# Performance work log

Hardware: AMD Instinct MI355X
Metric: run time of the kernel (lower is better)

## Reference

```python
import jax, jax.numpy as jnp
import numpy as np

B, NV, JN = 1024, 8, 21
V = NV * JN            # 168 tokens = num_view * joint_num
F_DIM, NH, DQ, DV = 512, 4, 128, 128
HID = 512
EPS = 1e-6
NEG = float(-2**32 + 1)


def _layer_norm(x, g, b):
    mu = jnp.mean(x, axis=-1, keepdims=True)
    var = jnp.mean(jnp.square(x - mu), axis=-1, keepdims=True)
    return (x - mu) * jax.lax.rsqrt(var + EPS) * g + b


def setup_inputs() -> dict:
    key = jax.random.key(0)
    ks = jax.random.split(key, 12)
    s = 0.02
    return {
        "x": jax.random.normal(ks[0], (B, V, F_DIM), dtype=jnp.float32),
        "valid": jax.random.randint(ks[1], (B, NV), 0, 2),
        "wq": jax.random.normal(ks[2], (NH * DQ, F_DIM), dtype=jnp.float32) * s,
        "bq": jnp.zeros((NH * DQ,), dtype=jnp.float32),
        "wk": jax.random.normal(ks[3], (NH * DQ, F_DIM), dtype=jnp.float32) * s,
        "bk": jnp.zeros((NH * DQ,), dtype=jnp.float32),
        "wv": jax.random.normal(ks[4], (NH * DV, F_DIM), dtype=jnp.float32) * s,
        "bv": jnp.zeros((NH * DV,), dtype=jnp.float32),
        "fc_w": jax.random.normal(ks[5], (F_DIM, NH * DV), dtype=jnp.float32) * s,
        "fc_b": jnp.zeros((F_DIM,), dtype=jnp.float32),
        "ln1_g": jnp.ones((F_DIM,), dtype=jnp.float32),
        "ln1_b": jnp.zeros((F_DIM,), dtype=jnp.float32),
        "ln2_g": jnp.ones((F_DIM,), dtype=jnp.float32),
        "ln2_b": jnp.zeros((F_DIM,), dtype=jnp.float32),
        "fc1_w": jax.random.normal(ks[6], (HID, F_DIM), dtype=jnp.float32) * s,
        "fc1_b": jnp.zeros((HID,), dtype=jnp.float32),
        "fc2_w": jax.random.normal(ks[7], (F_DIM, HID), dtype=jnp.float32) * s,
        "fc2_b": jnp.zeros((F_DIM,), dtype=jnp.float32),
    }


def reference(x, valid, wq, bq, wk, bk, wv, bv, fc_w, fc_b,
              ln1_g, ln1_b, ln2_g, ln2_b, fc1_w, fc1_b, fc2_w, fc2_b):
    bs = x.shape[0]
    h = _layer_norm(x, ln1_g, ln1_b)                          # [B,V,f]
    q = (h @ wq.T + bq).reshape(bs, V, NH, DQ)                # [B,V,H,dq]
    k = (h @ wk.T + bk).reshape(bs, V, NH, DQ)
    v = (h @ wv.T + bv).reshape(bs, V, NH, DV)
    attn = jnp.einsum('bqhd,bkhd->bhqk', q, k) / jnp.sqrt(jnp.float32(DQ))
    # valid mask: per-view validity expanded to per-token, pairwise additive
    w = jnp.where(valid == 0, NEG, 0.0).astype(x.dtype)       # [B,NV]
    w = jnp.repeat(w, JN, axis=1)                             # [B,V], view-major
    m = w[:, :, None] + w[:, None, :]                         # [B,V,V]
    attn = attn + m[:, None, :, :]
    attn = jax.nn.softmax(attn, axis=-1)
    out = jnp.einsum('bhqk,bkhd->bqhd', attn, v).reshape(bs, V, NH * DV)
    out = out @ fc_w.T + fc_b
    x = x + out
    # MLP residual block
    h2 = _layer_norm(x, ln2_g, ln2_b)
    h2 = jax.nn.relu(h2 @ fc1_w.T + fc1_b) @ fc2_w.T + fc2_b
    return x + h2
```

## Files before the change

kernel.cpp:

```cpp
#include <hip/hip_runtime.h>
#include <stdint.h>

#define BATCH 1024
#define NVIEW 8
#define JN_   21
#define VTOK  168
#define FDIM  512
#define NHEAD 4
#define DHEAD 128
#define MROWS (BATCH*VTOK)
#define SCALE2 0.127517434f

typedef __attribute__((ext_vector_type(8))) short s8v;
typedef __attribute__((ext_vector_type(4))) short s4v;
typedef __attribute__((ext_vector_type(4))) float f4v;

static __device__ __forceinline__ short f2bf(float f){
  unsigned u = __builtin_bit_cast(unsigned, f);
  unsigned r = (u + 0x7FFFu + ((u >> 16) & 1u)) >> 16;
  return (short)(unsigned short)r;
}
static __device__ __forceinline__ float bf2f(short s){
  unsigned u = ((unsigned)(unsigned short)s) << 16;
  return __builtin_bit_cast(float, u);
}

#define GL16(gp, lp) __builtin_amdgcn_global_load_lds( \
    (__attribute__((address_space(1))) void*)(gp), \
    (__attribute__((address_space(3))) void*)(lp), 16, 0, 0)

__global__ __launch_bounds__(256) void convert_w(
    const float* __restrict__ wq, const float* __restrict__ wk,
    const float* __restrict__ wv, const float* __restrict__ fcw,
    const float* __restrict__ fc1, const float* __restrict__ fc2,
    short* __restrict__ dst){
  int id = blockIdx.x * 256 + threadIdx.x;
  int e = id * 4;
  int seg = e >> 18;
  int off = e & 262143;
  const float* s = seg==0?wq: seg==1?wk: seg==2?wv: seg==3?fcw: seg==4?fc1: fc2;
  float4 u = *(const float4*)(s + off);
  s4v o; o[0]=f2bf(u.x); o[1]=f2bf(u.y); o[2]=f2bf(u.z); o[3]=f2bf(u.w);
  *(s4v*)(dst + e) = o;
}

__global__ __launch_bounds__(256) void ln1_kernel(
    const float* __restrict__ x, const float* __restrict__ g,
    const float* __restrict__ bb, short* __restrict__ h){
  int row  = blockIdx.x * 4 + (threadIdx.x >> 6);
  int lane = threadIdx.x & 63;
  size_t base = (size_t)row * 512 + lane * 8;
  float4 u0 = *(const float4*)(x + base);
  float4 u1 = *(const float4*)(x + base + 4);
  float s = u0.x+u0.y+u0.z+u0.w + u1.x+u1.y+u1.z+u1.w;
  float q = u0.x*u0.x+u0.y*u0.y+u0.z*u0.z+u0.w*u0.w
          + u1.x*u1.x+u1.y*u1.y+u1.z*u1.z+u1.w*u1.w;
  #pragma unroll
  for (int o = 1; o < 64; o <<= 1){ s += __shfl_xor(s,o); q += __shfl_xor(q,o); }
  float mu = s * (1.f/512.f);
  float rstd = rsqrtf(q*(1.f/512.f) - mu*mu + 1e-6f);
  float4 g0 = *(const float4*)(g + lane*8),  g1 = *(const float4*)(g + lane*8 + 4);
  float4 b0 = *(const float4*)(bb + lane*8), b1 = *(const float4*)(bb + lane*8 + 4);
  s8v o_;
  o_[0]=f2bf((u0.x-mu)*rstd*g0.x+b0.x); o_[1]=f2bf((u0.y-mu)*rstd*g0.y+b0.y);
  o_[2]=f2bf((u0.z-mu)*rstd*g0.z+b0.z); o_[3]=f2bf((u0.w-mu)*rstd*g0.w+b0.w);
  o_[4]=f2bf((u1.x-mu)*rstd*g1.x+b1.x); o_[5]=f2bf((u1.y-mu)*rstd*g1.y+b1.y);
  o_[6]=f2bf((u1.z-mu)*rstd*g1.z+b1.z); o_[7]=f2bf((u1.w-mu)*rstd*g1.w+b1.w);
  *(s8v*)(h + base) = o_;
}

__global__ __launch_bounds__(256) void resid_ln(
    const float* __restrict__ x, const short* __restrict__ y,
    const float* __restrict__ g, const float* __restrict__ bb,
    short* __restrict__ g2){
  int row  = blockIdx.x * 4 + (threadIdx.x >> 6);
  int lane = threadIdx.x & 63;
  size_t base = (size_t)row * 512 + lane * 8;
  float4 u0 = *(const float4*)(x + base);
  float4 u1 = *(const float4*)(x + base + 4);
  s8v yv = *(const s8v*)(y + base);
  float v[8];
  v[0]=u0.x+bf2f(yv[0]); v[1]=u0.y+bf2f(yv[1]); v[2]=u0.z+bf2f(yv[2]); v[3]=u0.w+bf2f(yv[3]);
  v[4]=u1.x+bf2f(yv[4]); v[5]=u1.y+bf2f(yv[5]); v[6]=u1.z+bf2f(yv[6]); v[7]=u1.w+bf2f(yv[7]);
  float s = 0.f, q = 0.f;
  #pragma unroll
  for (int i = 0; i < 8; i++){ s += v[i]; q += v[i]*v[i]; }
  #pragma unroll
  for (int o = 1; o < 64; o <<= 1){ s += __shfl_xor(s,o); q += __shfl_xor(q,o); }
  float mu = s * (1.f/512.f);
  float rstd = rsqrtf(q*(1.f/512.f) - mu*mu + 1e-6f);
  float4 g0 = *(const float4*)(g + lane*8),  g1 = *(const float4*)(g + lane*8 + 4);
  float4 b0 = *(const float4*)(bb + lane*8), b1 = *(const float4*)(bb + lane*8 + 4);
  s8v o_;
  o_[0]=f2bf((v[0]-mu)*rstd*g0.x+b0.x); o_[1]=f2bf((v[1]-mu)*rstd*g0.y+b0.y);
  o_[2]=f2bf((v[2]-mu)*rstd*g0.z+b0.z); o_[3]=f2bf((v[3]-mu)*rstd*g0.w+b0.w);
  o_[4]=f2bf((v[4]-mu)*rstd*g1.x+b1.x); o_[5]=f2bf((v[5]-mu)*rstd*g1.y+b1.y);
  o_[6]=f2bf((v[6]-mu)*rstd*g1.z+b1.z); o_[7]=f2bf((v[7]-mu)*rstd*g1.w+b1.w);
  *(s8v*)(g2 + base) = o_;
}

template<int MODE>
__global__ __launch_bounds__(512) void gemm_bt(
    const short* __restrict__ A, const short* __restrict__ Bm,
    const float* __restrict__ bias0, const float* __restrict__ bias1,
    const float* __restrict__ aux, short* __restrict__ out0,
    short* __restrict__ out1, float* __restrict__ outf){
  __shared__ short As[3][16384];
  __shared__ short Bs[3][8192];
  int tid = threadIdx.x, lane = tid & 63;
  int wid = tid >> 6, wr = wid >> 1, wc = wid & 1;
  int lg = lane >> 4, l15 = lane & 15;
  int nwg  = gridDim.x * gridDim.y;
  int flat = blockIdx.y * gridDim.x + blockIdx.x;
  int cpx  = nwg >> 3;
  int swz  = (flat & 7) * cpx + (flat >> 3);
  int bx = swz % gridDim.x, by = swz / gridDim.x;
  size_t mt, nt;
  if (MODE == 1){ mt = bx; nt = by; }
  else          { nt = bx; mt = by; }
  size_t m0 = mt * 256, n0 = nt * 128;
  const short* Ab = A + m0 * 512;
  const short* Bb = Bm + n0 * 512;
  f4v zf = {0.f,0.f,0.f,0.f};
  f4v acc[4][4];
  #pragma unroll
  for (int m=0;m<4;m++)
    #pragma unroll
    for (int n=0;n<4;n++) acc[m][n] = zf;

#define STAGE_T(bufi, kt) do {                                        \
    _Pragma("unroll")                                                 \
    for (int r_ = 0; r_ < 4; r_++){                                   \
      int c_ = r_*512 + tid;                                          \
      int row_ = c_ >> 3;                                             \
      int chk_ = (c_ & 7) ^ (row_ & 7);                               \
      GL16(Ab + (size_t)row_*512 + (kt) + chk_*8, &As[bufi][c_*8]);   \
    }                                                                 \
    _Pragma("unroll")                                                 \
    for (int r_ = 0; r_ < 2; r_++){                                   \
      int c_ = r_*512 + tid;                                          \
      int row_ = c_ >> 3;                                             \
      int chk_ = (c_ & 7) ^ (row_ & 7);                               \
      GL16(Bb + (size_t)row_*512 + (kt) + chk_*8, &Bs[bufi][c_*8]);   \
    }                                                                 \
  } while(0)

  STAGE_T(0, 0); STAGE_T(1, 64); STAGE_T(2, 128);

  #pragma unroll
  for (int t = 0; t < 8; ++t){
    if (t < 6)       asm volatile("s_waitcnt vmcnt(12)" ::: "memory");
    else if (t == 6) asm volatile("s_waitcnt vmcnt(6)"  ::: "memory");
    else             asm volatile("s_waitcnt vmcnt(0)"  ::: "memory");
    __builtin_amdgcn_s_barrier();
    __builtin_amdgcn_sched_barrier(0);
    {
      const short* Ap = As[t % 3];
      const short* Bp = Bs[t % 3];
      #pragma unroll
      for (int kk8 = 0; kk8 < 8; kk8 += 4){
        s8v af_[4], bf_[4];
        int pc_ = ((kk8 + lg) ^ (l15 & 7)) << 3;
        #pragma unroll
        for (int m_=0;m_<4;m_++) af_[m_] = *(const s8v*)&Ap[(wr*64+m_*16+l15)*64 + pc_];
        #pragma unroll
        for (int n_=0;n_<4;n_++) bf_[n_] = *(const s8v*)&Bp[(wc*64+n_*16+l15)*64 + pc_];
        __builtin_amdgcn_s_setprio(1);
        #pragma unroll
        for (int m_=0;m_<4;m_++)
          #pragma unroll
          for (int n_=0;n_<4;n_++)
            acc[m_][n_] = __builtin_amdgcn_mfma_f32_16x16x32_bf16(af_[m_], bf_[n_], acc[m_][n_], 0,0,0);
        __builtin_amdgcn_s_setprio(0);
      }
    }
    if (t < 5){
      __builtin_amdgcn_s_barrier();
      __builtin_amdgcn_sched_barrier(0);
      STAGE_T((t + 3) % 3, (t + 3) * 64);
    }
  }
#undef STAGE_T

  #pragma unroll
  for (int m=0;m<4;m++)
  #pragma unroll
  for (int n=0;n<4;n++)
  #pragma unroll
  for (int r=0;r<4;r++){
    int rowL = wr*64 + m*16 + lg*4 + r;
    int colL = wc*64 + n*16 + l15;
    size_t gm = m0 + rowL, gn = n0 + colL;
    float val = acc[m][n][r];
    if (MODE == 0){
      int nn = (int)gn;
      val += (nn < 512) ? bias0[nn] : bias1[nn - 512];
      int head = (nn >> 7) & 3, d = nn & 127;
      size_t b = gm / 168, tok = gm - b * 168;
      size_t idx = ((b*4 + head)*168 + tok)*128 + d;
      ((nn < 512) ? out0 : out1)[idx] = f2bf(val);
    } else if (MODE == 1){
      val += bias0[gm];
      int hh = ((int)gm >> 7) & 3, d = (int)gm & 127;
      size_t b = gn / 168, tok = gn - b * 168;
      out0[((b*4 + hh)*128 + d)*168 + tok] = f2bf(val);
    } else if (MODE == 2 || MODE == 3){
      val += bias0[gn];
      if (MODE == 3) val = fmaxf(val, 0.f);
      out0[gm*512 + gn] = f2bf(val);
    } else {
      val += bias0[gn] + aux[gm*512 + gn] + bf2f(out1[gm*512 + gn]);
      outf[gm*512 + gn] = val;
    }
  }
}

__global__ __launch_bounds__(256, 2) void attn_kernel(
    const short* __restrict__ qg_, const short* __restrict__ kg_,
    const short* __restrict__ vtg_, const int* __restrict__ valid,
    short* __restrict__ outp){
  __shared__ short Ps[192*200];

  int tid = threadIdx.x, lane = tid & 63, wid = tid >> 6;
  int lg = lane >> 4, l15 = lane & 15;
  int bh = blockIdx.x, b = bh >> 2, hh = bh & 3;
  const short* qg  = qg_  + (size_t)bh * (168*128);
  const short* kg  = kg_  + (size_t)bh * (168*128);
  const short* vtg = vtg_ + (size_t)bh * (128*168);

  int bits = 0;
  #pragma unroll
  for (int v = 0; v < 8; v++) bits |= (valid[b*8 + v] != 0) << v;
  if (bits == 0) bits = 255;
  float wk2[11];
  #pragma unroll
  for (int n = 0; n < 11; n++){
    int kt = n*16 + l15;
    int view = (kt * 781) >> 14;
    wk2[n] = ((bits >> view) & 1) ? 0.0f : -1.0e9f;
  }

  int row0 = wid * 48;
  f4v zf = {0.f,0.f,0.f,0.f};

  s8v qf[3][4];
  #pragma unroll
  for (int m=0;m<3;m++)
    #pragma unroll
    for (int kf=0;kf<4;kf++)
      qf[m][kf] = *(const s8v*)(qg + (size_t)(row0 + m*16 + l15)*128 + kf*32 + lg*8);

  f4v accS[3][11];
  #pragma unroll
  for (int m=0;m<3;m++)
    #pragma unroll
    for (int n=0;n<11;n++) accS[m][n] = zf;
  s8v kb[2][4];
  #pragma unroll
  for (int kf=0;kf<4;kf++)
    kb[0][kf] = *(const s8v*)(kg + (size_t)l15*128 + kf*32 + lg*8);
  #pragma unroll
  for (int n=0;n<11;n++){
    if (n < 10){
      #pragma unroll
      for (int kf=0;kf<4;kf++)
        kb[(n+1)&1][kf] = *(const s8v*)(kg + (size_t)((n+1)*16 + l15)*128 + kf*32 + lg*8);
    }
    __builtin_amdgcn_s_setprio(1);
    #pragma unroll
    for (int kf=0;kf<4;kf++)
      #pragma unroll
      for (int m=0;m<3;m++)
        accS[m][n] = __builtin_amdgcn_mfma_f32_16x16x32_bf16(qf[m][kf], kb[n&1][kf], accS[m][n], 0,0,0);
    __builtin_amdgcn_s_setprio(0);
  }

  float inv_[3][4];
  #pragma unroll
  for (int m=0;m<3;m++){
    #pragma unroll
    for (int r=0;r<4;r++){
      int qtok = row0 + m*16 + lg*4 + r;
      float sum = 0.f;
      #pragma unroll
      for (int n=0;n<11;n++){
        float p = exp2f(fmaf(accS[m][n][r], SCALE2, wk2[n]));
        sum += p;
        Ps[qtok*200 + n*16 + l15] = f2bf(p);
      }
      sum += __shfl_xor(sum,1); sum += __shfl_xor(sum,2);
      sum += __shfl_xor(sum,4); sum += __shfl_xor(sum,8);
      inv_[m][r] = 1.0f / sum;
    }
  }
  {
    s8v z8 = {0,0,0,0,0,0,0,0};
    for (int i = lane; i < 96; i += 64){
      int rr = row0 + (i >> 1);
      *(s8v*)&Ps[rr*200 + 176 + (i&1)*8] = z8;
    }
  }

  s8v ap[3][6];
  #pragma unroll
  for (int m=0;m<3;m++)
    #pragma unroll
    for (int kf=0;kf<6;kf++)
      ap[m][kf] = *(const s8v*)&Ps[(row0 + m*16 + l15)*200 + kf*32 + lg*8];

  f4v accO[3][8];
  #pragma unroll
  for (int m=0;m<3;m++)
    #pragma unroll
    for (int n=0;n<8;n++) accO[m][n] = zf;
  s8v vb[2][6];
  #pragma unroll
  for (int kf=0;kf<6;kf++)
    vb[0][kf] = *(const s8v*)(vtg + (size_t)l15*168 + kf*32 + lg*8);
  #pragma unroll
  for (int n=0;n<8;n++){
    if (n < 7){
      #pragma unroll
      for (int kf=0;kf<6;kf++)
        vb[(n+1)&1][kf] = *(const s8v*)(vtg + (size_t)((n+1)*16 + l15)*168 + kf*32 + lg*8);
    }
    __builtin_amdgcn_s_setprio(1);
    #pragma unroll
    for (int kf=0;kf<6;kf++)
      #pragma unroll
      for (int m=0;m<3;m++)
        accO[m][n] = __builtin_amdgcn_mfma_f32_16x16x32_bf16(ap[m][kf], vb[n&1][kf], accO[m][n], 0,0,0);
    __builtin_amdgcn_s_setprio(0);
  }

  #pragma unroll
  for (int m=0;m<3;m++){
    #pragma unroll
    for (int r=0;r<4;r++){
      int qtok = row0 + m*16 + lg*4 + r;
      if (qtok < 168){
        float iv = inv_[m][r];
        size_t base = ((size_t)b*168 + qtok)*512 + hh*128;
        #pragma unroll
        for (int n=0;n<8;n++)
          outp[base + n*16 + l15] = f2bf(accO[m][n][r] * iv);
      }
    }
  }
}

extern "C" void kernel_launch(void* const* d_in, const int* in_sizes, int n_in,
                              void* d_out, int out_size, void* d_ws, size_t ws_size,
                              hipStream_t stream) {
  const float* x     = (const float*)d_in[0];
  const int*   valid = (const int*)  d_in[1];
  const float* wq    = (const float*)d_in[2];
  const float* bq    = (const float*)d_in[3];
  const float* wk    = (const float*)d_in[4];
  const float* bk    = (const float*)d_in[5];
  const float* wv    = (const float*)d_in[6];
  const float* bv    = (const float*)d_in[7];
  const float* fcw   = (const float*)d_in[8];
  const float* fcb   = (const float*)d_in[9];
  const float* ln1g  = (const float*)d_in[10];
  const float* ln1b  = (const float*)d_in[11];
  const float* ln2g  = (const float*)d_in[12];
  const float* ln2b  = (const float*)d_in[13];
  const float* fc1w  = (const float*)d_in[14];
  const float* fc1b  = (const float*)d_in[15];
  const float* fc2w  = (const float*)d_in[16];
  const float* fc2b  = (const float*)d_in[17];

  char* ws = (char*)d_ws;
  short* h       = (short*)(ws + 0LL);
  short* q_ws    = (short*)(ws + 176160768LL);
  short* k_ws    = (short*)(ws + 352321536LL);
  short* vt_ws   = (short*)(ws + 528482304LL);
  short* wb      = (short*)(ws + 704643072LL);
  short* attn_o  = h;
  short* y       = q_ws;
  short* g2      = h;
  short* a1      = k_ws;
  float* outp    = (float*)d_out;

  convert_w<<<1536, 256, 0, stream>>>(wq, wk, wv, fcw, fc1w, fc2w, wb);
  ln1_kernel<<<MROWS/4, 256, 0, stream>>>(x, ln1g, ln1b, h);
  gemm_bt<0><<<dim3(8, MROWS/256), 512, 0, stream>>>(h, wb, bq, bk, nullptr, q_ws, k_ws, nullptr);
  gemm_bt<1><<<dim3(2, MROWS/128), 512, 0, stream>>>(wb + 524288, h, bv, nullptr, nullptr, vt_ws, nullptr, nullptr);
  attn_kernel<<<BATCH*NHEAD, 256, 0, stream>>>(q_ws, k_ws, vt_ws, valid, attn_o);
  gemm_bt<2><<<dim3(4, MROWS/256), 512, 0, stream>>>(attn_o, wb + 786432, fcb, nullptr, nullptr, y, nullptr, nullptr);
  resid_ln<<<MROWS/4, 256, 0, stream>>>(x, y, ln2g, ln2b, g2);
  gemm_bt<3><<<dim3(4, MROWS/256), 512, 0, stream>>>(g2, wb + 1048576, fc1b, nullptr, nullptr, a1, nullptr, nullptr);
  gemm_bt<4><<<dim3(4, MROWS/256), 512, 0, stream>>>(a1, wb + 1310720, fc2b, nullptr, (float*)x, nullptr, y, outp);
}
```

Measured before the change: 1.527 ms.

## Restructure GEMM pipeline to BK=32 triple-buffer, bf16 residual, deeper attention prefetch

The GEMM main loop moves from three 64-wide K stages with a split wait/stage schedule to sixteen 32-wide stages. Each stage loads its fragments, issues the next global-to-LDS copy, then runs MFMAs. LDS use drops so launch_bounds can request 4 blocks per SM. resid_ln now writes x+attn as bf16 so the final GEMM reads one bf16 residual instead of fp32 x plus bf16 y, cutting epilogue traffic at the cost of rounding the residual to bf16. The attention kernel's K and V fragment prefetch deepens from double to triple buffering, which costs more registers.

```diff
diff --git a/kernel.cpp b/kernel.cpp
--- a/kernel.cpp
+++ b/kernel.cpp
@@ -72,7 +72,7 @@
 __global__ __launch_bounds__(256) void resid_ln(
     const float* __restrict__ x, const short* __restrict__ y,
     const float* __restrict__ g, const float* __restrict__ bb,
-    short* __restrict__ g2){
+    short* __restrict__ x2b, short* __restrict__ g2){
   int row  = blockIdx.x * 4 + (threadIdx.x >> 6);
   int lane = threadIdx.x & 63;
   size_t base = (size_t)row * 512 + lane * 8;
@@ -82,6 +82,10 @@
   float v[8];
   v[0]=u0.x+bf2f(yv[0]); v[1]=u0.y+bf2f(yv[1]); v[2]=u0.z+bf2f(yv[2]); v[3]=u0.w+bf2f(yv[3]);
   v[4]=u1.x+bf2f(yv[4]); v[5]=u1.y+bf2f(yv[5]); v[6]=u1.z+bf2f(yv[6]); v[7]=u1.w+bf2f(yv[7]);
+  s8v xv;
+  #pragma unroll
+  for (int i = 0; i < 8; i++) xv[i] = f2bf(v[i]);
+  *(s8v*)(x2b + base) = xv;
   float s = 0.f, q = 0.f;
   #pragma unroll
   for (int i = 0; i < 8; i++){ s += v[i]; q += v[i]*v[i]; }
@@ -100,85 +104,76 @@
 }
 
 template<int MODE>
-__global__ __launch_bounds__(512) void gemm_bt(
+__global__ __launch_bounds__(512, 4) void gemm_bt(
     const short* __restrict__ A, const short* __restrict__ Bm,
     const float* __restrict__ bias0, const float* __restrict__ bias1,
-    const float* __restrict__ aux, short* __restrict__ out0,
+    const short* __restrict__ aux, short* __restrict__ out0,
     short* __restrict__ out1, float* __restrict__ outf){
-  __shared__ short As[3][16384];
-  __shared__ short Bs[3][8192];
-  int tid = threadIdx.x, lane = tid & 63;
-  int wid = tid >> 6, wr = wid >> 1, wc = wid & 1;
-  int lg = lane >> 4, l15 = lane & 15;
-  int nwg  = gridDim.x * gridDim.y;
-  int flat = blockIdx.y * gridDim.x + blockIdx.x;
-  int cpx  = nwg >> 3;
-  int swz  = (flat & 7) * cpx + (flat >> 3);
-  int bx = swz % gridDim.x, by = swz / gridDim.x;
+  __shared__ short lds[36864];
+  short* const AL = lds;
+  short* const BL = lds + 24576;
+  const int tid = threadIdx.x, lane = tid & 63;
+  const int wid = tid >> 6, wr = wid >> 1, wc = wid & 1;
+  const int lg = lane >> 4, l15 = lane & 15;
+  const int nwg  = gridDim.x * gridDim.y;
+  const int flat = blockIdx.y * gridDim.x + blockIdx.x;
+  const int swz  = (flat & 7) * (nwg >> 3) + (flat >> 3);
   size_t mt, nt;
-  if (MODE == 1){ mt = bx; nt = by; }
-  else          { nt = bx; mt = by; }
-  size_t m0 = mt * 256, n0 = nt * 128;
+  if (MODE == 1){ mt = swz & 1; nt = (size_t)(swz >> 1); }
+  else {
+    constexpr int GX = (MODE == 0) ? 8 : 4;
+    nt = swz % GX; mt = swz / GX;
+  }
+  const size_t m0 = mt * 256, n0 = nt * 128;
   const short* Ab = A + m0 * 512;
   const short* Bb = Bm + n0 * 512;
-  f4v zf = {0.f,0.f,0.f,0.f};
+
+#define STAGE_T(tt) do {                                                \
+    short* da_ = AL + ((tt)%3)*8192;                                    \
+    _Pragma("unroll")                                                   \
+    for (int r_ = 0; r_ < 2; r_++){                                     \
+      int c_ = r_*512 + tid;                                            \
+      int row_ = c_ >> 2, chk_ = (c_ & 3) ^ (row_ & 3);                 \
+      GL16(Ab + (size_t)row_*512 + (tt)*32 + chk_*8, da_ + c_*8);       \
+    }                                                                   \
+    {                                                                   \
+      short* db_ = BL + ((tt)%3)*4096;                                  \
+      int row_ = tid >> 2, chk_ = (tid & 3) ^ (row_ & 3);               \
+      GL16(Bb + (size_t)row_*512 + (tt)*32 + chk_*8, db_ + tid*8);      \
+    } } while(0)
+
+  STAGE_T(0); STAGE_T(1);
+  asm volatile("s_waitcnt vmcnt(3)" ::: "memory");
+  __builtin_amdgcn_s_barrier();
+
   f4v acc[4][4];
   #pragma unroll
   for (int m=0;m<4;m++)
     #pragma unroll
-    for (int n=0;n<4;n++) acc[m][n] = zf;
-
-#define STAGE_T(bufi, kt) do {                                        \
-    _Pragma("unroll")                                                 \
-    for (int r_ = 0; r_ < 4; r_++){                                   \
-      int c_ = r_*512 + tid;                                          \
-      int row_ = c_ >> 3;                                             \
-      int chk_ = (c_ & 7) ^ (row_ & 7);                               \
-      GL16(Ab + (size_t)row_*512 + (kt) + chk_*8, &As[bufi][c_*8]);   \
-    }                                                                 \
-    _Pragma("unroll")                                                 \
-    for (int r_ = 0; r_ < 2; r_++){                                   \
-      int c_ = r_*512 + tid;                                          \
-      int row_ = c_ >> 3;                                             \
-      int chk_ = (c_ & 7) ^ (row_ & 7);                               \
-      GL16(Bb + (size_t)row_*512 + (kt) + chk_*8, &Bs[bufi][c_*8]);   \
-    }                                                                 \
-  } while(0)
-
-  STAGE_T(0, 0); STAGE_T(1, 64); STAGE_T(2, 128);
-
-  #pragma unroll
-  for (int t = 0; t < 8; ++t){
-    if (t < 6)       asm volatile("s_waitcnt vmcnt(12)" ::: "memory");
-    else if (t == 6) asm volatile("s_waitcnt vmcnt(6)"  ::: "memory");
-    else             asm volatile("s_waitcnt vmcnt(0)"  ::: "memory");
+    for (int n=0;n<4;n++) acc[m][n] = f4v{0.f,0.f,0.f,0.f};
+
+  #pragma unroll
+  for (int t = 0; t < 16; ++t){
+    const short* Awp = AL + (t%3)*8192 + (wr*64 + l15)*32;
+    const short* Bwp = BL + (t%3)*4096 + (wc*64 + l15)*32;
+    const int cA = (lg ^ (l15 & 3)) * 8;
+    s8v af[4], bf[4];
+    #pragma unroll
+    for (int m=0;m<4;m++) af[m] = *(const s8v*)(Awp + m*512 + cA);
+    #pragma unroll
+    for (int n=0;n<4;n++) bf[n] = *(const s8v*)(Bwp + n*512 + cA);
+    if (t < 14) STAGE_T(t+2);
     __builtin_amdgcn_s_barrier();
-    __builtin_amdgcn_sched_barrier(0);
-    {
-      const short* Ap = As[t % 3];
-      const short* Bp = Bs[t % 3];
-      #pragma unroll
-      for (int kk8 = 0; kk8 < 8; kk8 += 4){
-        s8v af_[4], bf_[4];
-        int pc_ = ((kk8 + lg) ^ (l15 & 7)) << 3;
-        #pragma unroll
-        for (int m_=0;m_<4;m_++) af_[m_] = *(const s8v*)&Ap[(wr*64+m_*16+l15)*64 + pc_];
-        #pragma unroll
-        for (int n_=0;n_<4;n_++) bf_[n_] = *(const s8v*)&Bp[(wc*64+n_*16+l15)*64 + pc_];
-        __builtin_amdgcn_s_setprio(1);
-        #pragma unroll
-        for (int m_=0;m_<4;m_++)
-          #pragma unroll
-          for (int n_=0;n_<4;n_++)
-            acc[m_][n_] = __builtin_amdgcn_mfma_f32_16x16x32_bf16(af_[m_], bf_[n_], acc[m_][n_], 0,0,0);
-        __builtin_amdgcn_s_setprio(0);
-      }
-    }
-    if (t < 5){
-      __builtin_amdgcn_s_barrier();
-      __builtin_amdgcn_sched_barrier(0);
-      STAGE_T((t + 3) % 3, (t + 3) * 64);
-    }
+    __builtin_amdgcn_s_setprio(1);
+    #pragma unroll
+    for (int m=0;m<4;m++)
+      #pragma unroll
+      for (int n=0;n<4;n++)
+        acc[m][n] = __builtin_amdgcn_mfma_f32_16x16x32_bf16(af[m], bf[n], acc[m][n], 0,0,0);
+    __builtin_amdgcn_s_setprio(0);
+    if (t <= 13)      asm volatile("s_waitcnt vmcnt(3)" ::: "memory");
+    else if (t == 14) asm volatile("s_waitcnt vmcnt(0)" ::: "memory");
+    __builtin_amdgcn_s_barrier();
   }
 #undef STAGE_T
 
@@ -209,7 +204,7 @@
       if (MODE == 3) val = fmaxf(val, 0.f);
       out0[gm*512 + gn] = f2bf(val);
     } else {
-      val += bias0[gn] + aux[gm*512 + gn] + bf2f(out1[gm*512 + gn]);
+      val += bias0[gn] + bf2f(aux[gm*512 + gn]);
       outf[gm*512 + gn] = val;
     }
   }
@@ -255,23 +250,25 @@
   for (int m=0;m<3;m++)
     #pragma unroll
     for (int n=0;n<11;n++) accS[m][n] = zf;
-  s8v kb[2][4];
-  #pragma unroll
-  for (int kf=0;kf<4;kf++)
-    kb[0][kf] = *(const s8v*)(kg + (size_t)l15*128 + kf*32 + lg*8);
+  s8v kb[3][4];
+  #pragma unroll
+  for (int p=0;p<2;p++)
+    #pragma unroll
+    for (int kf=0;kf<4;kf++)
+      kb[p][kf] = *(const s8v*)(kg + (size_t)(p*16 + l15)*128 + kf*32 + lg*8);
   #pragma unroll
   for (int n=0;n<11;n++){
-    if (n < 10){
+    if (n < 9){
       #pragma unroll
       for (int kf=0;kf<4;kf++)
-        kb[(n+1)&1][kf] = *(const s8v*)(kg + (size_t)((n+1)*16 + l15)*128 + kf*32 + lg*8);
+        kb[(n+2)%3][kf] = *(const s8v*)(kg + (size_t)((n+2)*16 + l15)*128 + kf*32 + lg*8);
     }
     __builtin_amdgcn_s_setprio(1);
     #pragma unroll
     for (int kf=0;kf<4;kf++)
       #pragma unroll
       for (int m=0;m<3;m++)
-        accS[m][n] = __builtin_amdgcn_mfma_f32_16x16x32_bf16(qf[m][kf], kb[n&1][kf], accS[m][n], 0,0,0);
+        accS[m][n] = __builtin_amdgcn_mfma_f32_16x16x32_bf16(qf[m][kf], kb[n%3][kf], accS[m][n], 0,0,0);
     __builtin_amdgcn_s_setprio(0);
   }
 
@@ -313,23 +310,25 @@
   for (int m=0;m<3;m++)
     #pragma unroll
     for (int n=0;n<8;n++) accO[m][n] = zf;
-  s8v vb[2][6];
-  #pragma unroll
-  for (int kf=0;kf<6;kf++)
-    vb[0][kf] = *(const s8v*)(vtg + (size_t)l15*168 + kf*32 + lg*8);
+  s8v vb[3][6];
+  #pragma unroll
+  for (int p=0;p<2;p++)
+    #pragma unroll
+    for (int kf=0;kf<6;kf++)
+      vb[p][kf] = *(const s8v*)(vtg + (size_t)(p*16 + l15)*168 + kf*32 + lg*8);
   #pragma unroll
   for (int n=0;n<8;n++){
-    if (n < 7){
+    if (n < 6){
       #pragma unroll
       for (int kf=0;kf<6;kf++)
-        vb[(n+1)&1][kf] = *(const s8v*)(vtg + (size_t)((n+1)*16 + l15)*168 + kf*32 + lg*8);
+        vb[(n+2)%3][kf] = *(const s8v*)(vtg + (size_t)((n+2)*16 + l15)*168 + kf*32 + lg*8);
     }
     __builtin_amdgcn_s_setprio(1);
     #pragma unroll
     for (int kf=0;kf<6;kf++)
       #pragma unroll
       for (int m=0;m<3;m++)
-        accO[m][n] = __builtin_amdgcn_mfma_f32_16x16x32_bf16(ap[m][kf], vb[n&1][kf], accO[m][n], 0,0,0);
+        accO[m][n] = __builtin_amdgcn_mfma_f32_16x16x32_bf16(ap[m][kf], vb[n%3][kf], accO[m][n], 0,0,0);
     __builtin_amdgcn_s_setprio(0);
   }
 
@@ -381,6 +380,7 @@
   short* y       = q_ws;
   short* g2      = h;
   short* a1      = k_ws;
+  short* x2b     = vt_ws;
   float* outp    = (float*)d_out;
 
   convert_w<<<1536, 256, 0, stream>>>(wq, wk, wv, fcw, fc1w, fc2w, wb);
@@ -389,7 +389,7 @@
   gemm_bt<1><<<dim3(2, MROWS/128), 512, 0, stream>>>(wb + 524288, h, bv, nullptr, nullptr, vt_ws, nullptr, nullptr);
   attn_kernel<<<BATCH*NHEAD, 256, 0, stream>>>(q_ws, k_ws, vt_ws, valid, attn_o);
   gemm_bt<2><<<dim3(4, MROWS/256), 512, 0, stream>>>(attn_o, wb + 786432, fcb, nullptr, nullptr, y, nullptr, nullptr);
-  resid_ln<<<MROWS/4, 256, 0, stream>>>(x, y, ln2g, ln2b, g2);
+  resid_ln<<<MROWS/4, 256, 0, stream>>>(x, y, ln2g, ln2b, x2b, g2);
   gemm_bt<3><<<dim3(4, MROWS/256), 512, 0, stream>>>(g2, wb + 1048576, fc1b, nullptr, nullptr, a1, nullptr, nullptr);
-  gemm_bt<4><<<dim3(4, MROWS/256), 512, 0, stream>>>(a1, wb + 1310720, fc2b, nullptr, (float*)x, nullptr, y, outp);
-}
+  gemm_bt<4><<<dim3(4, MROWS/256), 512, 0, stream>>>(a1, wb + 1310720, fc2b, nullptr, x2b, nullptr, nullptr, outp);
+}
```

After: 1.346 ms. -11.8%, faster.
